# Kernel tuning notes

Hardware: AMD Instinct MI355X
Metric: run time of the kernel (lower is better)

Reference implementation:

```python
import jax, jax.numpy as jnp
import numpy as np

TEMPERATURE = 0.07
EPS = 1e-12  # F.normalize default eps


def setup_inputs() -> dict:
    key = jax.random.key(0)
    k1, k2, k3 = jax.random.split(key, 3)
    B, C, H, W = 2, 128, 256, 256
    return {
        "z1": jax.random.normal(k1, (B, C, H, W), dtype=jnp.float32),
        "z2": jax.random.normal(k2, (B, C, H, W), dtype=jnp.float32),
        "labels": jax.random.randint(k3, (B, H, W), 0, 5),
        "chunks": 64,
    }


def _l2_normalize(x, axis):
    n = jnp.sqrt(jnp.sum(x * x, axis=axis, keepdims=True))
    return x / jnp.maximum(n, EPS)


def reference(z1, z2, labels, chunks):
    B, C, H, W = z1.shape
    N = H * W
    M = N // chunks  # chunk length (N divisible by chunks)

    # normalize over channel dim, flatten spatial, split into chunks: [B, C, K, M]
    z1c = _l2_normalize(z1, axis=1).reshape(B, C, N).reshape(B, C, chunks, M)
    z2c = _l2_normalize(z2, axis=1).reshape(B, C, N).reshape(B, C, chunks, M)
    lab = labels.reshape(B, N).reshape(B, chunks, M)  # [B, K, M]

    # positives: cosine sim between matching chunks of z1 and z2 (unit vectors -> dot)
    pos = jnp.einsum("bckm,bckm->bkm", z1c, z2c) / TEMPERATURE  # [B, K, M]

    # negatives: in the source, (reps2, l2) after the j-loop are the LAST chunk of z2
    reps2_last = z2c[:, :, -1, :]  # [B, C, M]
    l2_last = lab[:, -1, :]        # [B, M]

    neg = jnp.einsum("bckm,bcn->bkmn", z1c, reps2_last)  # [B, K, M, M]
    mask = (lab[:, :, :, None] != l2_last[:, None, None, :])  # True where labels differ
    neg = neg * mask / TEMPERATURE

    logits = jnp.concatenate([pos[..., None], neg], axis=-1)  # [B, K, M, M+1]
    logp = jax.nn.log_softmax(logits, axis=-1)

    # per-(b,chunk) term is -mean over [M, M+1]; final is mean over B*chunks terms
    return -jnp.mean(logp)
```

## Files before the change

kernel.cpp:

```cpp
#include <hip/hip_runtime.h>
#include <hip/hip_bf16.h>

constexpr int BB = 2;
constexpr int CC = 128;
constexpr int NN = 65536;
constexpr int MM = 1024;
constexpr int LASTOFF = 63 * 1024;
constexpr float INV_T = 1.0f / 0.07f;
constexpr float L2E = 1.44269504088896340736f;
constexpr float C2 = INV_T * L2E;
constexpr float SCALE = 1.0f / (134348800.0f * 1.44269504088896340736f);
constexpr float EPSN = 1e-12f;

typedef float f32x4 __attribute__((ext_vector_type(4)));
typedef short bf16x8 __attribute__((ext_vector_type(8)));

__device__ __forceinline__ uint pack_bf16(float a, float b) {
  __hip_bfloat16 ha = __float2bfloat16(a);
  __hip_bfloat16 hb = __float2bfloat16(b);
  ushort ua = *reinterpret_cast<ushort*>(&ha);
  ushort ub = *reinterpret_cast<ushort*>(&hb);
  return (uint)ua | ((uint)ub << 16);
}

__global__ __launch_bounds__(256) void k_pos(
    const float* __restrict__ z1, const float* __restrict__ z2,
    float* __restrict__ i1c2, float* __restrict__ posv) {
  const int b = blockIdx.y;
  const int px = blockIdx.x * 512 + 2 * threadIdx.x;
  const float* p1 = z1 + (size_t)b * CC * NN + px;
  const float* p2 = z2 + (size_t)b * CC * NN + px;
  float s11a = 0.f, s22a = 0.f, s12a = 0.f;
  float s11b = 0.f, s22b = 0.f, s12b = 0.f;
#pragma unroll 8
  for (int c = 0; c < CC; c++) {
    float2 x = *reinterpret_cast<const float2*>(p1 + (size_t)c * NN);
    float2 y = *reinterpret_cast<const float2*>(p2 + (size_t)c * NN);
    s11a += x.x * x.x; s22a += y.x * y.x; s12a += x.x * y.x;
    s11b += x.y * x.y; s22b += y.y * y.y; s12b += x.y * y.y;
  }
  float i1a = 1.0f / fmaxf(sqrtf(s11a), EPSN);
  float i2a = 1.0f / fmaxf(sqrtf(s22a), EPSN);
  float i1b = 1.0f / fmaxf(sqrtf(s11b), EPSN);
  float i2b = 1.0f / fmaxf(sqrtf(s22b), EPSN);
  float2 iv = {i1a * C2, i1b * C2};
  float2 pv = {s12a * i1a * i2a * C2, s12b * i1b * i2b * C2};
  *reinterpret_cast<float2*>(i1c2 + (size_t)b * NN + px) = iv;
  *reinterpret_cast<float2*>(posv + (size_t)b * NN + px) = pv;
}

__global__ __launch_bounds__(256) void k_r2(
    const float* __restrict__ z2, const int* __restrict__ lab,
    uint* __restrict__ r2n, float* __restrict__ Sv) {
  __shared__ float t2[64 * 129];
  __shared__ float part[8][65];
  __shared__ float inv2s[64];
  __shared__ int cls[64];
  const int b = blockIdx.y;
  const int pg = blockIdx.x * 64;
  const int p0 = LASTOFF + pg;
  const int t = threadIdx.x;
  const int p2 = t & 31;
  const int q = t >> 5;
  const float* s2 = z2 + (size_t)b * CC * NN + p0 + 2 * p2;
  float a22 = 0.f, b22 = 0.f;
#pragma unroll
  for (int e = 0; e < 16; e++) {
    int c = e * 8 + q;
    float2 y = *reinterpret_cast<const float2*>(s2 + (size_t)c * NN);
    t2[(2 * p2) * 129 + c] = y.x;
    t2[(2 * p2 + 1) * 129 + c] = y.y;
    a22 += y.x * y.x;
    b22 += y.y * y.y;
  }
  part[q][2 * p2] = a22;
  part[q][2 * p2 + 1] = b22;
  __syncthreads();
  if (t < 64) {
    float s22 = 0.f;
#pragma unroll
    for (int qq = 0; qq < 8; qq++) s22 += part[qq][t];
    inv2s[t] = 1.0f / fmaxf(sqrtf(s22), EPSN);
    cls[t] = lab[(size_t)b * NN + p0 + t];
  }
  __syncthreads();
  const size_t obase = ((size_t)b * MM + pg) * 64;
#pragma unroll
  for (int e = 0; e < 16; e++) {
    int lin = e * 256 + t;
    int pp = lin >> 6;
    int cp = lin & 63;
    float i2 = inv2s[pp];
    float v0 = t2[pp * 129 + 2 * cp] * i2;
    float v1 = t2[pp * 129 + 2 * cp + 1] * i2;
    r2n[obase + (size_t)pp * 64 + cp] = pack_bf16(v0, v1);
  }
  const int c = t & 127;
  const int h = t >> 7;
  float tot = 0.f, se0 = 0.f, se1 = 0.f, se2 = 0.f, se3 = 0.f, se4 = 0.f;
#pragma unroll
  for (int k = 0; k < 32; k++) {
    int pp = h * 32 + k;
    float val = t2[pp * 129 + c] * inv2s[pp];
    int lb = cls[pp];
    tot += val;
    se0 += (lb == 0) ? val : 0.f;
    se1 += (lb == 1) ? val : 0.f;
    se2 += (lb == 2) ? val : 0.f;
    se3 += (lb == 3) ? val : 0.f;
    se4 += (lb == 4) ? val : 0.f;
  }
  float* svb = Sv + b * 640 + c;
  atomicAdd(svb + 0 * 128, tot - se0);
  atomicAdd(svb + 1 * 128, tot - se1);
  atomicAdd(svb + 2 * 128, tot - se2);
  atomicAdd(svb + 3 * 128, tot - se3);
  atomicAdd(svb + 4 * 128, tot - se4);
}

__global__ void k_svpack(const float* __restrict__ Sv, ushort* __restrict__ r2x) {
  int i = blockIdx.x * 256 + threadIdx.x;
  if (i >= BB * 16 * 128) return;
  int b = i >> 11, rr = (i >> 7) & 15, c = i & 127;
  float v = (rr < 5) ? Sv[b * 640 + rr * 128 + c] : 0.0f;
  __hip_bfloat16 h = __float2bfloat16(v);
  r2x[i] = *reinterpret_cast<ushort*>(&h);
}

__global__ __launch_bounds__(256) void k_gemm(
    const float* __restrict__ z1, const float* __restrict__ i1c2,
    const ushort* __restrict__ r2n, const ushort* __restrict__ r2x,
    const int* __restrict__ lab, const float* __restrict__ posv,
    float* __restrict__ accum) {
  __shared__ ushort At[128 * 258];
  const int b = blockIdx.y;
  const int px0 = blockIdx.x * 256;
  const int tid = threadIdx.x;
  const int w = tid >> 6;
  const int lane = tid & 63;
  const int r = lane & 15;
  const int kg = lane >> 4;

  {
    const float* zb = z1 + (size_t)b * CC * NN + px0 + 4 * lane;
    f32x4 iv = *reinterpret_cast<const f32x4*>(i1c2 + (size_t)b * NN + px0 + 4 * lane);
#pragma unroll 4
    for (int e = 0; e < 32; e++) {
      int c = w * 32 + e;
      f32x4 v = *reinterpret_cast<const f32x4*>(zb + (size_t)c * NN);
      uint2 uu;
      uu.x = pack_bf16(v[0] * iv[0], v[1] * iv[1]);
      uu.y = pack_bf16(v[2] * iv[2], v[3] * iv[3]);
      *reinterpret_cast<uint2*>(&At[c * 258 + 4 * lane]) = uu;
    }
  }
  __syncthreads();

  const int wrow0 = w * 64;
  bf16x8 av[4][4];
#pragma unroll
  for (int g = 0; g < 4; g++)
#pragma unroll
    for (int kk = 0; kk < 4; kk++) {
      bf16x8 tv;
#pragma unroll
      for (int j = 0; j < 8; j++)
        tv[j] = (short)At[(kg * 8 + kk * 32 + j) * 258 + wrow0 + g * 16 + r];
      av[g][kk] = tv;
    }

  int rl[16];
#pragma unroll
  for (int g = 0; g < 4; g++)
#pragma unroll
    for (int i = 0; i < 4; i++)
      rl[g * 4 + i] = lab[(size_t)b * NN + px0 + wrow0 + g * 16 + kg * 4 + i];

  float sAcc[16];
#pragma unroll
  for (int s = 0; s < 16; s++) sAcc[s] = 0.f;

  const ushort* Bbase = r2n + (size_t)b * MM * CC;
  const int* clbase = lab + (size_t)b * NN + LASTOFF;

#pragma unroll 1
  for (int ch = 0; ch < 16; ch++) {
    const int n0 = ch * 64;
    bf16x8 bv[4][4];
#pragma unroll
    for (int tt = 0; tt < 4; tt++)
#pragma unroll
      for (int kk = 0; kk < 4; kk++)
        bv[tt][kk] = *reinterpret_cast<const bf16x8*>(
            Bbase + ((size_t)(n0 + tt * 16 + r)) * CC + kg * 8 + kk * 32);
    int cl[4];
#pragma unroll
    for (int tt = 0; tt < 4; tt++)
      cl[tt] = clbase[n0 + tt * 16 + r];

    f32x4 acc[4][4];
#pragma unroll
    for (int g = 0; g < 4; g++)
#pragma unroll
      for (int tt = 0; tt < 4; tt++)
        acc[g][tt] = f32x4{0.f, 0.f, 0.f, 0.f};

#pragma unroll
    for (int kk = 0; kk < 4; kk++)
#pragma unroll
      for (int g = 0; g < 4; g++)
#pragma unroll
        for (int tt = 0; tt < 4; tt++)
          acc[g][tt] = __builtin_amdgcn_mfma_f32_16x16x32_bf16(
              av[g][kk], bv[tt][kk], acc[g][tt], 0, 0, 0);

#pragma unroll
    for (int g = 0; g < 4; g++)
#pragma unroll
      for (int tt = 0; tt < 4; tt++)
#pragma unroll
        for (int i = 0; i < 4; i++) {
          float xm = (rl[g * 4 + i] != cl[tt]) ? acc[g][tt][i] : 0.0f;
          sAcc[g * 4 + i] += __builtin_amdgcn_exp2f(xm);
        }
  }

  f32x4 accx[4];
  {
    bf16x8 bx[4];
#pragma unroll
    for (int kk = 0; kk < 4; kk++)
      bx[kk] = *reinterpret_cast<const bf16x8*>(
          r2x + (size_t)b * 16 * CC + (size_t)r * CC + kg * 8 + kk * 32);
#pragma unroll
    for (int g = 0; g < 4; g++) {
      accx[g] = f32x4{0.f, 0.f, 0.f, 0.f};
#pragma unroll
      for (int kk = 0; kk < 4; kk++)
        accx[g] = __builtin_amdgcn_mfma_f32_16x16x32_bf16(
            av[g][kk], bx[kk], accx[g], 0, 0, 0);
    }
  }

#pragma unroll
  for (int d = 1; d < 16; d <<= 1)
#pragma unroll
    for (int s = 0; s < 16; s++) sAcc[s] += __shfl_xor(sAcc[s], d);

  float xsel[16];
#pragma unroll
  for (int g = 0; g < 4; g++)
#pragma unroll
    for (int i = 0; i < 4; i++)
      xsel[g * 4 + i] = __shfl(accx[g][i], (lane & 48) | rl[g * 4 + i]);

  float tv = 0.f;
  if (r == 0) {
#pragma unroll
    for (int g = 0; g < 4; g++)
#pragma unroll
      for (int i = 0; i < 4; i++) {
        int row = px0 + wrow0 + g * 16 + kg * 4 + i;
        float pv = posv[(size_t)b * NN + row];
        float s = sAcc[g * 4 + i] + __builtin_amdgcn_exp2f(pv);
        float x = xsel[g * 4 + i] + pv;
        tv += 1025.0f * __log2f(s) - x;
      }
  }
  tv += __shfl_xor(tv, 16);
  tv += __shfl_xor(tv, 32);
  if (lane == 0) atomicAdd(accum, tv);
}

__global__ void k_scale(const float* __restrict__ accum, float* __restrict__ out) {
  out[0] = accum[0] * SCALE;
}

extern "C" void kernel_launch(void* const* d_in, const int* in_sizes, int n_in,
                              void* d_out, int out_size, void* d_ws, size_t ws_size,
                              hipStream_t stream) {
  const float* z1 = (const float*)d_in[0];
  const float* z2 = (const float*)d_in[1];
  const int* lab = (const int*)d_in[2];

  char* ws = (char*)d_ws;
  uint* r2n   = (uint*)ws;
  ushort* r2x = (ushort*)(ws + 524288);
  float* posv = (float*)(ws + 532480);
  float* i1c2 = (float*)(ws + 1056768);
  float* Sv   = (float*)(ws + 1581056);
  float* accum = (float*)(ws + 1586176);

  hipMemsetAsync(ws + 1581056, 0, 5124, stream);

  k_pos<<<dim3(NN / 512, BB), 256, 0, stream>>>(z1, z2, i1c2, posv);
  k_r2<<<dim3(MM / 64, BB), 256, 0, stream>>>(z2, lab, r2n, Sv);
  k_svpack<<<dim3(16), 256, 0, stream>>>(Sv, r2x);
  k_gemm<<<dim3(NN / 256, BB), 256, 0, stream>>>(
      z1, i1c2, (const ushort*)r2n, r2x, lab, posv, accum);
  k_scale<<<1, 1, 0, stream>>>(accum, (float*)d_out);
}
```

Measured before the change: 253.6 us.

## Halve gemm row tile to 128 rows, cut registers for higher occupancy

The fused similarity/logsumexp kernel now handles 128 rows per block instead of 256, with each wave owning 32 rows. The MFMA inner loop is restructured to process one 16-column B tile at a time, so far fewer accumulator and B-fragment registers are live, and launch bounds request 4 blocks per CU. The z1 staging loads now use float2 with channel-interleaved waves, and the position kernel's channel loop is unrolled further. The tradeoff is twice as many blocks, each reloading the full B matrix (r2n) from cache, so the B reuse per load is halved.

```diff
diff --git a/kernel.cpp b/kernel.cpp
--- a/kernel.cpp
+++ b/kernel.cpp
@@ -32,7 +32,7 @@
   const float* p2 = z2 + (size_t)b * CC * NN + px;
   float s11a = 0.f, s22a = 0.f, s12a = 0.f;
   float s11b = 0.f, s22b = 0.f, s12b = 0.f;
-#pragma unroll 8
+#pragma unroll 16
   for (int c = 0; c < CC; c++) {
     float2 x = *reinterpret_cast<const float2*>(p1 + (size_t)c * NN);
     float2 y = *reinterpret_cast<const float2*>(p2 + (size_t)c * NN);
@@ -127,14 +127,14 @@
   r2x[i] = *reinterpret_cast<ushort*>(&h);
 }
 
-__global__ __launch_bounds__(256) void k_gemm(
+__global__ __launch_bounds__(256, 4) void k_gemm(
     const float* __restrict__ z1, const float* __restrict__ i1c2,
     const ushort* __restrict__ r2n, const ushort* __restrict__ r2x,
     const int* __restrict__ lab, const float* __restrict__ posv,
     float* __restrict__ accum) {
-  __shared__ ushort At[128 * 258];
+  __shared__ ushort At[128 * 130];
   const int b = blockIdx.y;
-  const int px0 = blockIdx.x * 256;
+  const int px0 = blockIdx.x * 128;
   const int tid = threadIdx.x;
   const int w = tid >> 6;
   const int lane = tid & 63;
@@ -142,114 +142,103 @@
   const int kg = lane >> 4;
 
   {
-    const float* zb = z1 + (size_t)b * CC * NN + px0 + 4 * lane;
-    f32x4 iv = *reinterpret_cast<const f32x4*>(i1c2 + (size_t)b * NN + px0 + 4 * lane);
-#pragma unroll 4
+    const int pxl = 2 * (tid & 63);
+    const int cg = tid >> 6;
+    const float* zb = z1 + (size_t)b * CC * NN + px0 + pxl;
+    float2 iv = *reinterpret_cast<const float2*>(i1c2 + (size_t)b * NN + px0 + pxl);
+#pragma unroll
     for (int e = 0; e < 32; e++) {
-      int c = w * 32 + e;
-      f32x4 v = *reinterpret_cast<const f32x4*>(zb + (size_t)c * NN);
-      uint2 uu;
-      uu.x = pack_bf16(v[0] * iv[0], v[1] * iv[1]);
-      uu.y = pack_bf16(v[2] * iv[2], v[3] * iv[3]);
-      *reinterpret_cast<uint2*>(&At[c * 258 + 4 * lane]) = uu;
+      int c = e * 4 + cg;
+      float2 v = *reinterpret_cast<const float2*>(zb + (size_t)c * NN);
+      *reinterpret_cast<uint*>(&At[c * 130 + pxl]) = pack_bf16(v.x * iv.x, v.y * iv.y);
     }
   }
   __syncthreads();
 
-  const int wrow0 = w * 64;
-  bf16x8 av[4][4];
-#pragma unroll
-  for (int g = 0; g < 4; g++)
+  const int wrow0 = w * 32;
+  bf16x8 av[2][4];
+#pragma unroll
+  for (int g = 0; g < 2; g++)
 #pragma unroll
     for (int kk = 0; kk < 4; kk++) {
       bf16x8 tv;
 #pragma unroll
       for (int j = 0; j < 8; j++)
-        tv[j] = (short)At[(kg * 8 + kk * 32 + j) * 258 + wrow0 + g * 16 + r];
+        tv[j] = (short)At[(kg * 8 + kk * 32 + j) * 130 + wrow0 + g * 16 + r];
       av[g][kk] = tv;
     }
 
-  int rl[16];
-#pragma unroll
-  for (int g = 0; g < 4; g++)
+  int rl[8];
+#pragma unroll
+  for (int g = 0; g < 2; g++)
 #pragma unroll
     for (int i = 0; i < 4; i++)
       rl[g * 4 + i] = lab[(size_t)b * NN + px0 + wrow0 + g * 16 + kg * 4 + i];
 
-  float sAcc[16];
-#pragma unroll
-  for (int s = 0; s < 16; s++) sAcc[s] = 0.f;
+  float sAcc[8];
+#pragma unroll
+  for (int s = 0; s < 8; s++) sAcc[s] = 0.f;
 
   const ushort* Bbase = r2n + (size_t)b * MM * CC;
   const int* clbase = lab + (size_t)b * NN + LASTOFF;
 
-#pragma unroll 1
+#pragma unroll
   for (int ch = 0; ch < 16; ch++) {
     const int n0 = ch * 64;
-    bf16x8 bv[4][4];
-#pragma unroll
-    for (int tt = 0; tt < 4; tt++)
-#pragma unroll
-      for (int kk = 0; kk < 4; kk++)
-        bv[tt][kk] = *reinterpret_cast<const bf16x8*>(
-            Bbase + ((size_t)(n0 + tt * 16 + r)) * CC + kg * 8 + kk * 32);
-    int cl[4];
-#pragma unroll
-    for (int tt = 0; tt < 4; tt++)
-      cl[tt] = clbase[n0 + tt * 16 + r];
-
-    f32x4 acc[4][4];
-#pragma unroll
-    for (int g = 0; g < 4; g++)
-#pragma unroll
-      for (int tt = 0; tt < 4; tt++)
-        acc[g][tt] = f32x4{0.f, 0.f, 0.f, 0.f};
-
-#pragma unroll
-    for (int kk = 0; kk < 4; kk++)
-#pragma unroll
-      for (int g = 0; g < 4; g++)
-#pragma unroll
-        for (int tt = 0; tt < 4; tt++)
-          acc[g][tt] = __builtin_amdgcn_mfma_f32_16x16x32_bf16(
-              av[g][kk], bv[tt][kk], acc[g][tt], 0, 0, 0);
-
-#pragma unroll
-    for (int g = 0; g < 4; g++)
-#pragma unroll
-      for (int tt = 0; tt < 4; tt++)
-#pragma unroll
-        for (int i = 0; i < 4; i++) {
-          float xm = (rl[g * 4 + i] != cl[tt]) ? acc[g][tt][i] : 0.0f;
-          sAcc[g * 4 + i] += __builtin_amdgcn_exp2f(xm);
-        }
-  }
-
-  f32x4 accx[4];
+#pragma unroll
+    for (int tt = 0; tt < 4; tt++) {
+      const ushort* Bt = Bbase + (size_t)(n0 + tt * 16 + r) * CC + kg * 8;
+      bf16x8 bv0 = *reinterpret_cast<const bf16x8*>(Bt);
+      bf16x8 bv1 = *reinterpret_cast<const bf16x8*>(Bt + 32);
+      bf16x8 bv2 = *reinterpret_cast<const bf16x8*>(Bt + 64);
+      bf16x8 bv3 = *reinterpret_cast<const bf16x8*>(Bt + 96);
+      int cl = clbase[n0 + tt * 16 + r];
+      f32x4 a0 = {0.f, 0.f, 0.f, 0.f};
+      f32x4 a1 = {0.f, 0.f, 0.f, 0.f};
+      a0 = __builtin_amdgcn_mfma_f32_16x16x32_bf16(av[0][0], bv0, a0, 0, 0, 0);
+      a1 = __builtin_amdgcn_mfma_f32_16x16x32_bf16(av[1][0], bv0, a1, 0, 0, 0);
+      a0 = __builtin_amdgcn_mfma_f32_16x16x32_bf16(av[0][1], bv1, a0, 0, 0, 0);
+      a1 = __builtin_amdgcn_mfma_f32_16x16x32_bf16(av[1][1], bv1, a1, 0, 0, 0);
+      a0 = __builtin_amdgcn_mfma_f32_16x16x32_bf16(av[0][2], bv2, a0, 0, 0, 0);
+      a1 = __builtin_amdgcn_mfma_f32_16x16x32_bf16(av[1][2], bv2, a1, 0, 0, 0);
+      a0 = __builtin_amdgcn_mfma_f32_16x16x32_bf16(av[0][3], bv3, a0, 0, 0, 0);
+      a1 = __builtin_amdgcn_mfma_f32_16x16x32_bf16(av[1][3], bv3, a1, 0, 0, 0);
+#pragma unroll
+      for (int i = 0; i < 4; i++) {
+        float x0 = (rl[i] != cl) ? a0[i] : 0.0f;
+        float x1 = (rl[4 + i] != cl) ? a1[i] : 0.0f;
+        sAcc[i] += __builtin_amdgcn_exp2f(x0);
+        sAcc[4 + i] += __builtin_amdgcn_exp2f(x1);
+      }
+    }
+  }
+
+  f32x4 accx[2];
   {
-    bf16x8 bx[4];
-#pragma unroll
-    for (int kk = 0; kk < 4; kk++)
-      bx[kk] = *reinterpret_cast<const bf16x8*>(
-          r2x + (size_t)b * 16 * CC + (size_t)r * CC + kg * 8 + kk * 32);
-#pragma unroll
-    for (int g = 0; g < 4; g++) {
-      accx[g] = f32x4{0.f, 0.f, 0.f, 0.f};
-#pragma unroll
-      for (int kk = 0; kk < 4; kk++)
-        accx[g] = __builtin_amdgcn_mfma_f32_16x16x32_bf16(
-            av[g][kk], bx[kk], accx[g], 0, 0, 0);
+    const ushort* Bx = r2x + (size_t)b * 16 * CC + (size_t)r * CC + kg * 8;
+    bf16x8 bx0 = *reinterpret_cast<const bf16x8*>(Bx);
+    bf16x8 bx1 = *reinterpret_cast<const bf16x8*>(Bx + 32);
+    bf16x8 bx2 = *reinterpret_cast<const bf16x8*>(Bx + 64);
+    bf16x8 bx3 = *reinterpret_cast<const bf16x8*>(Bx + 96);
+#pragma unroll
+    for (int g = 0; g < 2; g++) {
+      f32x4 ax = {0.f, 0.f, 0.f, 0.f};
+      ax = __builtin_amdgcn_mfma_f32_16x16x32_bf16(av[g][0], bx0, ax, 0, 0, 0);
+      ax = __builtin_amdgcn_mfma_f32_16x16x32_bf16(av[g][1], bx1, ax, 0, 0, 0);
+      ax = __builtin_amdgcn_mfma_f32_16x16x32_bf16(av[g][2], bx2, ax, 0, 0, 0);
+      ax = __builtin_amdgcn_mfma_f32_16x16x32_bf16(av[g][3], bx3, ax, 0, 0, 0);
+      accx[g] = ax;
     }
   }
 
 #pragma unroll
   for (int d = 1; d < 16; d <<= 1)
 #pragma unroll
-    for (int s = 0; s < 16; s++) sAcc[s] += __shfl_xor(sAcc[s], d);
-
-  float xsel[16];
-#pragma unroll
-  for (int g = 0; g < 4; g++)
+    for (int s = 0; s < 8; s++) sAcc[s] += __shfl_xor(sAcc[s], d);
+
+  float xsel[8];
+#pragma unroll
+  for (int g = 0; g < 2; g++)
 #pragma unroll
     for (int i = 0; i < 4; i++)
       xsel[g * 4 + i] = __shfl(accx[g][i], (lane & 48) | rl[g * 4 + i]);
@@ -257,7 +246,7 @@
   float tv = 0.f;
   if (r == 0) {
 #pragma unroll
-    for (int g = 0; g < 4; g++)
+    for (int g = 0; g < 2; g++)
 #pragma unroll
       for (int i = 0; i < 4; i++) {
         int row = px0 + wrow0 + g * 16 + kg * 4 + i;
@@ -296,7 +285,7 @@
   k_pos<<<dim3(NN / 512, BB), 256, 0, stream>>>(z1, z2, i1c2, posv);
   k_r2<<<dim3(MM / 64, BB), 256, 0, stream>>>(z2, lab, r2n, Sv);
   k_svpack<<<dim3(16), 256, 0, stream>>>(Sv, r2x);
-  k_gemm<<<dim3(NN / 256, BB), 256, 0, stream>>>(
+  k_gemm<<<dim3(NN / 128, BB), 256, 0, stream>>>(
       z1, i1c2, (const ushort*)r2n, r2x, lab, posv, accum);
   k_scale<<<1, 1, 0, stream>>>(accum, (float*)d_out);
 }
```

Measured after the change: 340.0 us. +34.1%, slower.

## Split GEMM over column halves with single-wave blocks and separate loss kernel

Applied to the files above, without the earlier changes.

The GEMM kernel changes from 256-thread blocks that stage the normalized z1 tile in LDS to 64-thread single-wave blocks. Each block loads its A fragments straight from global memory and handles one half of the 1024 negatives, so the grid has many more blocks. Partial exp-sums and the selected class dot products go to workspace buffers, and a new reduction kernel computes the log terms. k_pos also splits the channel loop across four wave groups and reduces through LDS, which raises block count and parallelism. The cost is uncoalesced strided global loads for the A fragments, z1 being read twice (once per half), and an extra kernel launch with intermediate memory traffic.

```diff
diff --git a/kernel.cpp b/kernel.cpp
--- a/kernel.cpp
+++ b/kernel.cpp
@@ -26,27 +26,36 @@
 __global__ __launch_bounds__(256) void k_pos(
     const float* __restrict__ z1, const float* __restrict__ z2,
     float* __restrict__ i1c2, float* __restrict__ posv) {
+  __shared__ float part[3][4][132];
   const int b = blockIdx.y;
-  const int px = blockIdx.x * 512 + 2 * threadIdx.x;
-  const float* p1 = z1 + (size_t)b * CC * NN + px;
-  const float* p2 = z2 + (size_t)b * CC * NN + px;
+  const int px0 = blockIdx.x * 128;
+  const int t = threadIdx.x;
+  const int g = t >> 6;
+  const int pr = 2 * (t & 63);
+  const float* p1 = z1 + (size_t)b * CC * NN + (size_t)(g * 32) * NN + px0 + pr;
+  const float* p2 = z2 + (size_t)b * CC * NN + (size_t)(g * 32) * NN + px0 + pr;
   float s11a = 0.f, s22a = 0.f, s12a = 0.f;
   float s11b = 0.f, s22b = 0.f, s12b = 0.f;
-#pragma unroll 8
-  for (int c = 0; c < CC; c++) {
-    float2 x = *reinterpret_cast<const float2*>(p1 + (size_t)c * NN);
-    float2 y = *reinterpret_cast<const float2*>(p2 + (size_t)c * NN);
+#pragma unroll
+  for (int e = 0; e < 32; e++) {
+    float2 x = *reinterpret_cast<const float2*>(p1 + (size_t)e * NN);
+    float2 y = *reinterpret_cast<const float2*>(p2 + (size_t)e * NN);
     s11a += x.x * x.x; s22a += y.x * y.x; s12a += x.x * y.x;
     s11b += x.y * x.y; s22b += y.y * y.y; s12b += x.y * y.y;
   }
-  float i1a = 1.0f / fmaxf(sqrtf(s11a), EPSN);
-  float i2a = 1.0f / fmaxf(sqrtf(s22a), EPSN);
-  float i1b = 1.0f / fmaxf(sqrtf(s11b), EPSN);
-  float i2b = 1.0f / fmaxf(sqrtf(s22b), EPSN);
-  float2 iv = {i1a * C2, i1b * C2};
-  float2 pv = {s12a * i1a * i2a * C2, s12b * i1b * i2b * C2};
-  *reinterpret_cast<float2*>(i1c2 + (size_t)b * NN + px) = iv;
-  *reinterpret_cast<float2*>(posv + (size_t)b * NN + px) = pv;
+  part[0][g][pr] = s11a; part[0][g][pr + 1] = s11b;
+  part[1][g][pr] = s22a; part[1][g][pr + 1] = s22b;
+  part[2][g][pr] = s12a; part[2][g][pr + 1] = s12b;
+  __syncthreads();
+  if (t < 128) {
+    float s11 = part[0][0][t] + part[0][1][t] + part[0][2][t] + part[0][3][t];
+    float s22 = part[1][0][t] + part[1][1][t] + part[1][2][t] + part[1][3][t];
+    float s12 = part[2][0][t] + part[2][1][t] + part[2][2][t] + part[2][3][t];
+    float i1 = 1.0f / fmaxf(sqrtf(s11), EPSN);
+    float i2 = 1.0f / fmaxf(sqrtf(s22), EPSN);
+    i1c2[(size_t)b * NN + px0 + t] = i1 * C2;
+    posv[(size_t)b * NN + px0 + t] = s12 * i1 * i2 * C2;
+  }
 }
 
 __global__ __launch_bounds__(256) void k_r2(
@@ -127,149 +136,150 @@
   r2x[i] = *reinterpret_cast<ushort*>(&h);
 }
 
-__global__ __launch_bounds__(256) void k_gemm(
+__global__ __launch_bounds__(64) void k_gemm(
     const float* __restrict__ z1, const float* __restrict__ i1c2,
     const ushort* __restrict__ r2n, const ushort* __restrict__ r2x,
-    const int* __restrict__ lab, const float* __restrict__ posv,
-    float* __restrict__ accum) {
-  __shared__ ushort At[128 * 258];
-  const int b = blockIdx.y;
-  const int px0 = blockIdx.x * 256;
-  const int tid = threadIdx.x;
-  const int w = tid >> 6;
-  const int lane = tid & 63;
+    const int* __restrict__ lab, float* __restrict__ sp,
+    float* __restrict__ xp) {
+  const int b = blockIdx.z;
+  const int half = blockIdx.y;
+  const int px0 = blockIdx.x * 64;
+  const int lane = threadIdx.x;
   const int r = lane & 15;
   const int kg = lane >> 4;
-
-  {
-    const float* zb = z1 + (size_t)b * CC * NN + px0 + 4 * lane;
-    f32x4 iv = *reinterpret_cast<const f32x4*>(i1c2 + (size_t)b * NN + px0 + 4 * lane);
-#pragma unroll 4
-    for (int e = 0; e < 32; e++) {
-      int c = w * 32 + e;
-      f32x4 v = *reinterpret_cast<const f32x4*>(zb + (size_t)c * NN);
-      uint2 uu;
-      uu.x = pack_bf16(v[0] * iv[0], v[1] * iv[1]);
-      uu.y = pack_bf16(v[2] * iv[2], v[3] * iv[3]);
-      *reinterpret_cast<uint2*>(&At[c * 258 + 4 * lane]) = uu;
-    }
-  }
-  __syncthreads();
-
-  const int wrow0 = w * 64;
+  const size_t bN = (size_t)b * NN;
+
   bf16x8 av[4][4];
 #pragma unroll
+  for (int g = 0; g < 4; g++) {
+    const int px = px0 + g * 16 + r;
+    const float iv = i1c2[bN + px];
+    const float* zc = z1 + bN * CC + px;
+#pragma unroll
+    for (int kk = 0; kk < 4; kk++) {
+      const int c0 = kk * 32 + kg * 8;
+      bf16x8 tv;
+#pragma unroll
+      for (int j = 0; j < 8; j++) {
+        float v = zc[(size_t)(c0 + j) * NN] * iv;
+        __hip_bfloat16 h = __float2bfloat16(v);
+        tv[j] = *reinterpret_cast<short*>(&h);
+      }
+      av[g][kk] = tv;
+    }
+  }
+
+  int rl[16];
+#pragma unroll
   for (int g = 0; g < 4; g++)
 #pragma unroll
-    for (int kk = 0; kk < 4; kk++) {
-      bf16x8 tv;
-#pragma unroll
-      for (int j = 0; j < 8; j++)
-        tv[j] = (short)At[(kg * 8 + kk * 32 + j) * 258 + wrow0 + g * 16 + r];
-      av[g][kk] = tv;
-    }
-
-  int rl[16];
-#pragma unroll
-  for (int g = 0; g < 4; g++)
-#pragma unroll
     for (int i = 0; i < 4; i++)
-      rl[g * 4 + i] = lab[(size_t)b * NN + px0 + wrow0 + g * 16 + kg * 4 + i];
+      rl[g * 4 + i] = lab[bN + px0 + g * 16 + kg * 4 + i];
 
   float sAcc[16];
 #pragma unroll
   for (int s = 0; s < 16; s++) sAcc[s] = 0.f;
 
-  const ushort* Bbase = r2n + (size_t)b * MM * CC;
-  const int* clbase = lab + (size_t)b * NN + LASTOFF;
-
-#pragma unroll 1
-  for (int ch = 0; ch < 16; ch++) {
-    const int n0 = ch * 64;
-    bf16x8 bv[4][4];
-#pragma unroll
-    for (int tt = 0; tt < 4; tt++)
+  const ushort* Bh = r2n + ((size_t)b * MM + half * 512) * CC;
+  const int* clbase = lab + bN + LASTOFF + half * 512;
+
+#pragma unroll 2
+  for (int nc = 0; nc < 16; nc++) {
+    const int n0 = nc * 32;
+    bf16x8 bv[2][4];
+    int cl[2];
+#pragma unroll
+    for (int tt = 0; tt < 2; tt++) {
+      const ushort* Bt = Bh + (size_t)(n0 + tt * 16 + r) * CC + kg * 8;
 #pragma unroll
       for (int kk = 0; kk < 4; kk++)
-        bv[tt][kk] = *reinterpret_cast<const bf16x8*>(
-            Bbase + ((size_t)(n0 + tt * 16 + r)) * CC + kg * 8 + kk * 32);
-    int cl[4];
-#pragma unroll
-    for (int tt = 0; tt < 4; tt++)
+        bv[tt][kk] = *reinterpret_cast<const bf16x8*>(Bt + kk * 32);
       cl[tt] = clbase[n0 + tt * 16 + r];
-
-    f32x4 acc[4][4];
+    }
+    f32x4 acc[4][2];
 #pragma unroll
     for (int g = 0; g < 4; g++)
 #pragma unroll
-      for (int tt = 0; tt < 4; tt++)
+      for (int tt = 0; tt < 2; tt++)
         acc[g][tt] = f32x4{0.f, 0.f, 0.f, 0.f};
-
 #pragma unroll
     for (int kk = 0; kk < 4; kk++)
 #pragma unroll
       for (int g = 0; g < 4; g++)
 #pragma unroll
-        for (int tt = 0; tt < 4; tt++)
+        for (int tt = 0; tt < 2; tt++)
           acc[g][tt] = __builtin_amdgcn_mfma_f32_16x16x32_bf16(
               av[g][kk], bv[tt][kk], acc[g][tt], 0, 0, 0);
-
 #pragma unroll
     for (int g = 0; g < 4; g++)
 #pragma unroll
-      for (int tt = 0; tt < 4; tt++)
+      for (int tt = 0; tt < 2; tt++)
 #pragma unroll
         for (int i = 0; i < 4; i++) {
-          float xm = (rl[g * 4 + i] != cl[tt]) ? acc[g][tt][i] : 0.0f;
-          sAcc[g * 4 + i] += __builtin_amdgcn_exp2f(xm);
+          float x = (rl[g * 4 + i] != cl[tt]) ? acc[g][tt][i] : 0.0f;
+          sAcc[g * 4 + i] += __builtin_amdgcn_exp2f(x);
         }
   }
 
-  f32x4 accx[4];
-  {
+#pragma unroll
+  for (int d = 1; d < 16; d <<= 1)
+#pragma unroll
+    for (int s = 0; s < 16; s++) sAcc[s] += __shfl_xor(sAcc[s], d);
+
+  if (r == 0) {
+#pragma unroll
+    for (int s = 0; s < 16; s++) {
+      int row = px0 + (s >> 2) * 16 + kg * 4 + (s & 3);
+      sp[(size_t)half * (BB * (size_t)NN) + bN + row] = sAcc[s];
+    }
+  }
+
+  if (half == 0) {
     bf16x8 bx[4];
+    const ushort* Bx = r2x + (size_t)b * 16 * CC + (size_t)r * CC + kg * 8;
 #pragma unroll
     for (int kk = 0; kk < 4; kk++)
-      bx[kk] = *reinterpret_cast<const bf16x8*>(
-          r2x + (size_t)b * 16 * CC + (size_t)r * CC + kg * 8 + kk * 32);
+      bx[kk] = *reinterpret_cast<const bf16x8*>(Bx + kk * 32);
+    f32x4 accx[4];
 #pragma unroll
     for (int g = 0; g < 4; g++) {
-      accx[g] = f32x4{0.f, 0.f, 0.f, 0.f};
+      f32x4 ax = {0.f, 0.f, 0.f, 0.f};
 #pragma unroll
       for (int kk = 0; kk < 4; kk++)
-        accx[g] = __builtin_amdgcn_mfma_f32_16x16x32_bf16(
-            av[g][kk], bx[kk], accx[g], 0, 0, 0);
-    }
-  }
-
-#pragma unroll
-  for (int d = 1; d < 16; d <<= 1)
-#pragma unroll
-    for (int s = 0; s < 16; s++) sAcc[s] += __shfl_xor(sAcc[s], d);
-
-  float xsel[16];
-#pragma unroll
-  for (int g = 0; g < 4; g++)
-#pragma unroll
-    for (int i = 0; i < 4; i++)
-      xsel[g * 4 + i] = __shfl(accx[g][i], (lane & 48) | rl[g * 4 + i]);
-
-  float tv = 0.f;
-  if (r == 0) {
+        ax = __builtin_amdgcn_mfma_f32_16x16x32_bf16(av[g][kk], bx[kk], ax, 0, 0, 0);
+      accx[g] = ax;
+    }
+    float xsel[16];
 #pragma unroll
     for (int g = 0; g < 4; g++)
 #pragma unroll
-      for (int i = 0; i < 4; i++) {
-        int row = px0 + wrow0 + g * 16 + kg * 4 + i;
-        float pv = posv[(size_t)b * NN + row];
-        float s = sAcc[g * 4 + i] + __builtin_amdgcn_exp2f(pv);
-        float x = xsel[g * 4 + i] + pv;
-        tv += 1025.0f * __log2f(s) - x;
+      for (int i = 0; i < 4; i++)
+        xsel[g * 4 + i] = __shfl(accx[g][i], (lane & 48) | rl[g * 4 + i]);
+    if (r == 0) {
+#pragma unroll
+      for (int s = 0; s < 16; s++) {
+        int row = px0 + (s >> 2) * 16 + kg * 4 + (s & 3);
+        xp[bN + row] = xsel[s];
       }
-  }
-  tv += __shfl_xor(tv, 16);
-  tv += __shfl_xor(tv, 32);
-  if (lane == 0) atomicAdd(accum, tv);
+    }
+  }
+}
+
+__global__ __launch_bounds__(256) void k_loss(
+    const float* __restrict__ sp, const float* __restrict__ xp,
+    const float* __restrict__ posv, float* __restrict__ accum) {
+  __shared__ float red[4];
+  const int idx = blockIdx.x * 256 + threadIdx.x;
+  float pv = posv[idx];
+  float s = sp[idx] + sp[BB * (size_t)NN + idx] + __builtin_amdgcn_exp2f(pv);
+  float x = xp[idx] + pv;
+  float tv = 1025.0f * __log2f(s) - x;
+#pragma unroll
+  for (int d = 1; d < 64; d <<= 1) tv += __shfl_xor(tv, d);
+  if ((threadIdx.x & 63) == 0) red[threadIdx.x >> 6] = tv;
+  __syncthreads();
+  if (threadIdx.x == 0)
+    atomicAdd(accum, red[0] + red[1] + red[2] + red[3]);
 }
 
 __global__ void k_scale(const float* __restrict__ accum, float* __restrict__ out) {
@@ -290,13 +300,16 @@
   float* i1c2 = (float*)(ws + 1056768);
   float* Sv   = (float*)(ws + 1581056);
   float* accum = (float*)(ws + 1586176);
+  float* sp   = (float*)(ws + 1589248);
+  float* xp   = (float*)(ws + 2637824);
 
   hipMemsetAsync(ws + 1581056, 0, 5124, stream);
 
-  k_pos<<<dim3(NN / 512, BB), 256, 0, stream>>>(z1, z2, i1c2, posv);
+  k_pos<<<dim3(NN / 128, BB), 256, 0, stream>>>(z1, z2, i1c2, posv);
   k_r2<<<dim3(MM / 64, BB), 256, 0, stream>>>(z2, lab, r2n, Sv);
   k_svpack<<<dim3(16), 256, 0, stream>>>(Sv, r2x);
-  k_gemm<<<dim3(NN / 256, BB), 256, 0, stream>>>(
-      z1, i1c2, (const ushort*)r2n, r2x, lab, posv, accum);
+  k_gemm<<<dim3(NN / 64, 2, BB), 64, 0, stream>>>(
+      z1, i1c2, (const ushort*)r2n, r2x, lab, sp, xp);
+  k_loss<<<dim3(BB * NN / 256), 256, 0, stream>>>(sp, xp, posv, accum);
   k_scale<<<1, 1, 0, stream>>>(accum, (float*)d_out);
 }
```

Measured after the change: 284.8 us. 12.3% more time.
